# Kernel tuning notes

Hardware: AMD Instinct MI355X
Metric: run time of the kernel (lower is better)

Reference implementation:

```python
import jax, jax.numpy as jnp
import numpy as np

CODEBOOK_SIZE = 2048
LATENT_DIM = 256
COMMITMENT_BETA = 0.25
B, C, T = 16, LATENT_DIM, 2048


def setup_inputs() -> dict:
    key = jax.random.key(0)
    k1, k2 = jax.random.split(key)
    x = jax.random.normal(k1, (B, C, T), dtype=jnp.float32)
    # matches nn.Embedding.weight.data.uniform_(-1/K, 1/K)
    codebook = jax.random.uniform(
        k2, (CODEBOOK_SIZE, LATENT_DIM), dtype=jnp.float32,
        minval=-1.0 / CODEBOOK_SIZE, maxval=1.0 / CODEBOOK_SIZE)
    return {"x": x, "codebook": codebook}


def reference(x, codebook):
    b, c, t = x.shape
    # (B, C, T) -> (B*T, C)
    xf = jnp.transpose(x, (0, 2, 1)).reshape(b * t, c)
    # squared Euclidean distances; argmin is invariant to the sqrt in torch.cdist(p=2)
    x_sq = jnp.sum(xf * xf, axis=1, keepdims=True)            # (BT, 1)
    e_sq = jnp.sum(codebook * codebook, axis=1)[None, :]      # (1, K)
    d2 = x_sq - 2.0 * (xf @ codebook.T) + e_sq                # (BT, K)
    idx = jnp.argmin(d2, axis=-1)                             # (BT,)
    # gather codebook vectors -> (B, C, T)
    quant = codebook[idx].reshape(b, t, c).transpose(0, 2, 1)
    commitment_loss = COMMITMENT_BETA * jnp.mean(
        (jax.lax.stop_gradient(quant) - x) ** 2)
    codebook_loss = jnp.mean((quant - jax.lax.stop_gradient(x)) ** 2)
    # straight-through estimator
    quant_out = x + jax.lax.stop_gradient(quant - x)
    return quant_out, codebook_loss, commitment_loss, idx.reshape(b, t)
```

## Files before the change

### kernel.cpp

```cpp
#include <hip/hip_runtime.h>
#include <hip/hip_bf16.h>

#define KCODES 2048
#define DIM 256
#define TLEN 2048
#define NB 16
#define NROWS (NB * TLEN)
#define NELEM (NB * DIM * TLEN)
#define LOSS_OFF NELEM
#define IDX_OFF (NELEM + 2)

#define AMARGIN 1.8e-3f

#define CCAP 48

#define OFF_XSQ   0ull
#define OFF_ESQ   131072ull
#define OFF_KEYS  139264ull
#define OFF_BSUM  401408ull
#define OFF_EHI   532480ull
#define OFF_CCNT  1581056ull
#define OFF_CLIST 1712128ull
#define WS_NEED   8003584ull

typedef __bf16 bf16x8 __attribute__((ext_vector_type(8)));
typedef float  f32x4  __attribute__((ext_vector_type(4)));
typedef int    i32x4  __attribute__((ext_vector_type(4)));

__device__ __forceinline__ float sq_rn(float v) { return __fmul_rn(v, v); }

__device__ __forceinline__ unsigned encf(float f) {
    unsigned u = __float_as_uint(f);
    return (u & 0x80000000u) ? ~u : (u | 0x80000000u);
}
__device__ __forceinline__ float decf(unsigned k) {
    return __uint_as_float((k & 0x80000000u) ? (k & 0x7FFFFFFFu) : ~k);
}

__global__ __launch_bounds__(256) void xsq_kernel(const float* __restrict__ x,
                                                  float* __restrict__ xsq) {
    int m = blockIdx.x * 256 + threadIdx.x;
    int b = m >> 11, t = m & (TLEN - 1);
    const float* p = x + (size_t)b * DIM * TLEN + t;
    float h[2];
#pragma unroll
    for (int half = 0; half < 2; ++half) {
        int c0 = half * 128;
        float r[8];
#pragma unroll
        for (int j = 0; j < 8; ++j) r[j] = sq_rn(p[(size_t)(c0 + j) * TLEN]);
        for (int i = 8; i < 128; i += 8) {
#pragma unroll
            for (int j = 0; j < 8; ++j)
                r[j] = __fadd_rn(r[j], sq_rn(p[(size_t)(c0 + i + j) * TLEN]));
        }
        h[half] = __fadd_rn(__fadd_rn(__fadd_rn(r[0], r[1]), __fadd_rn(r[2], r[3])),
                            __fadd_rn(__fadd_rn(r[4], r[5]), __fadd_rn(r[6], r[7])));
    }
    xsq[m] = __fadd_rn(h[0], h[1]);
}

__global__ __launch_bounds__(256) void esq_kernel(const float* __restrict__ cb,
                                                  float* __restrict__ esq) {
    int k = blockIdx.x * 256 + threadIdx.x;
    const float* p = cb + (size_t)k * DIM;
    float h[2];
#pragma unroll
    for (int half = 0; half < 2; ++half) {
        int c0 = half * 128;
        float r[8];
#pragma unroll
        for (int j = 0; j < 8; ++j) r[j] = sq_rn(p[c0 + j]);
        for (int i = 8; i < 128; i += 8) {
#pragma unroll
            for (int j = 0; j < 8; ++j)
                r[j] = __fadd_rn(r[j], sq_rn(p[c0 + i + j]));
        }
        h[half] = __fadd_rn(__fadd_rn(__fadd_rn(r[0], r[1]), __fadd_rn(r[2], r[3])),
                            __fadd_rn(__fadd_rn(r[4], r[5]), __fadd_rn(r[6], r[7])));
    }
    esq[k] = __fadd_rn(h[0], h[1]);
}

__global__ __launch_bounds__(256) void prep_e_kernel(const float* __restrict__ cb,
                                                     __hip_bfloat16* __restrict__ Ehi,
                                                     float* __restrict__ esq) {
    int tid = threadIdx.x;
    int w = tid >> 6, lane = tid & 63;
    int k = (blockIdx.x << 2) + w;
    const float* p = cb + (size_t)k * DIM;

    float4 v = *reinterpret_cast<const float4*>(p + (lane << 2));
    alignas(8) __hip_bfloat16 h4[4];
    h4[0] = __float2bfloat16(v.x); h4[1] = __float2bfloat16(v.y);
    h4[2] = __float2bfloat16(v.z); h4[3] = __float2bfloat16(v.w);
    *reinterpret_cast<int2*>(Ehi + (size_t)k * DIM + (lane << 2)) = *reinterpret_cast<int2*>(h4);

    if (lane < 16) {
        int c0 = (lane >> 3) << 7, j = lane & 7;
        float r = sq_rn(p[c0 + j]);
        for (int i = 8; i < 128; i += 8)
            r = __fadd_rn(r, sq_rn(p[c0 + i + j]));
        float a  = __fadd_rn(r,  __shfl_xor(r, 1, 16));
        float b2 = __fadd_rn(a,  __shfl_xor(a, 2, 16));
        float h  = __fadd_rn(b2, __shfl_xor(b2, 4, 16));
        float tot = __fadd_rn(h, __shfl_xor(h, 8, 16));
        if (lane == 0) esq[k] = tot;
    }
}

__device__ __forceinline__ void stage_chunk(const __hip_bfloat16* __restrict__ Ehi,
                                            __hip_bfloat16* dstbase,
                                            int s, int w, int srow, int scol) {
    int ntq = s >> 3, half = (s >> 2) & 1, kc = s & 3;
    const __hip_bfloat16* gsrc =
        Ehi + (size_t)((ntq << 7) + (half << 6) + (w << 4) + srow) * DIM + (kc << 6) + scol;
#pragma unroll
    for (int j = 0; j < 2; ++j)
        __builtin_amdgcn_global_load_lds(
            (const __attribute__((address_space(1))) unsigned int*)(gsrc + (size_t)(j << 3) * DIM),
            (__attribute__((address_space(3))) unsigned int*)(dstbase + (((w << 4) + (j << 3)) << 6)),
            16, 0, 0);
}

__global__ __launch_bounds__(256, 2) void dist_cand_kernel(const float* __restrict__ x,
                                                           const __hip_bfloat16* __restrict__ Ehi,
                                                           int* __restrict__ ccnt_g,
                                                           int* __restrict__ clist_g) {
    __shared__ __hip_bfloat16 Bh[3][64 * 64];
    __shared__ unsigned short wmax16_s[64][66];
    __shared__ unsigned mask_s[64][65];
    __shared__ int ccnt_s[64];

    int tid = threadIdx.x;
    int w = tid >> 6, lane = tid & 63;
    int q = lane >> 4, c = lane & 15;
    int swzc = (c & 7) << 4;
    int blk = blockIdx.x;
    int b = blk >> 5;
    int t0 = (blk << 6) & (TLEN - 1);
    const float* xb = x + (size_t)b * DIM * TLEN + t0;

    if (tid < 64) ccnt_s[tid] = 0;

    i32x4 xf[4][8];
#pragma unroll
    for (int mi = 0; mi < 4; ++mi) {
        int t = (mi << 4) + c;
#pragma unroll
        for (int kh = 0; kh < 8; ++kh) {
            union { __hip_bfloat16 h[8]; i32x4 v; } u;
#pragma unroll
            for (int j = 0; j < 8; ++j)
                u.h[j] = __float2bfloat16(xb[(size_t)((kh << 5) + (q << 3) + j) * TLEN + t]);
            xf[mi][kh] = u.v;
            asm volatile("" : "+v"(xf[mi][kh]));
        }
    }

    f32x4 acc[2][4];
#pragma unroll
    for (int ci = 0; ci < 2; ++ci)
#pragma unroll
        for (int mi = 0; mi < 4; ++mi) acc[ci][mi] = (f32x4){0.f, 0.f, 0.f, 0.f};

    int srow = lane >> 3;
    int scol = ((lane & 7) ^ srow) << 3;

    asm volatile("s_waitcnt vmcnt(0)" ::: "memory");

    stage_chunk(Ehi, &Bh[0][0], 0, w, srow, scol);
    stage_chunk(Ehi, &Bh[1][0], 1, w, srow, scol);

    int cur = 0;
#pragma unroll 1
    for (int nt = 0; nt < 16; ++nt) {
#pragma unroll
        for (int hk = 0; hk < 8; ++hk) {
            int s = (nt << 3) + hk;
            int half = (hk >> 2) & 1;
            asm volatile("s_waitcnt lgkmcnt(0)" ::: "memory");
            int sb = cur == 0 ? 2 : cur - 1;
            if (s + 2 < 128) stage_chunk(Ehi, &Bh[sb][0], s + 2, w, srow, scol);
            if (s < 126) asm volatile("s_waitcnt vmcnt(4)" ::: "memory");
            else         asm volatile("s_waitcnt vmcnt(0)" ::: "memory");

            const char* basep = reinterpret_cast<const char*>(&Bh[cur][0]);
            int rowbyte = ((w << 4) + c) << 7;
#pragma unroll
            for (int kh = 0; kh < 2; ++kh) {
                int swz = ((kh << 6) | (q << 4)) ^ swzc;
                bf16x8 cf = *reinterpret_cast<const bf16x8*>(basep + rowbyte + swz);
#pragma unroll
                for (int mi = 0; mi < 4; ++mi) {
                    bf16x8 af = __builtin_bit_cast(bf16x8, xf[mi][((hk & 3) << 1) | kh]);
                    acc[half][mi] = __builtin_amdgcn_mfma_f32_16x16x32_bf16(cf, af, acc[half][mi], 0, 0, 0);
                }
            }
            cur = cur == 2 ? 0 : cur + 1;
        }

#pragma unroll
        for (int mi = 0; mi < 4; ++mi) {
            int r = (mi << 4) + c;
            float a8[8];
#pragma unroll
            for (int ci = 0; ci < 2; ++ci)
#pragma unroll
                for (int reg = 0; reg < 4; ++reg)
                    a8[ci * 4 + reg] = acc[ci][mi][reg];
            float m01 = fmaxf(fmaxf(a8[0], a8[1]), fmaxf(a8[2], a8[3]));
            float m23 = fmaxf(fmaxf(a8[4], a8[5]), fmaxf(a8[6], a8[7]));
            float wmax = fmaxf(m01, m23);
            wmax = fmaxf(wmax, __shfl_xor(wmax, 16, 64));
            wmax = fmaxf(wmax, __shfl_xor(wmax, 32, 64));
            float thrw = wmax - AMARGIN;
            unsigned bits = 0;
#pragma unroll
            for (int v = 0; v < 8; ++v)
                if (a8[v] >= thrw)
                    bits |= 1u << (((v >> 2) << 4) | (q << 2) | (v & 3));
            bits |= (unsigned)__shfl_xor((int)bits, 16, 64);
            bits |= (unsigned)__shfl_xor((int)bits, 32, 64);
            if (q == 0) {
                int st = (nt << 2) | w;
                wmax16_s[r][st] = (unsigned short)(encf(wmax) >> 16);
                mask_s[r][st] = bits;
            }
            acc[0][mi] = (f32x4){0.f, 0.f, 0.f, 0.f};
            acc[1][mi] = (f32x4){0.f, 0.f, 0.f, 0.f};
        }
    }

    __syncthreads();

    {
        int r = tid >> 2, j4 = tid & 3;
        int m = (blk << 6) + r;
        int g16 = 0;
#pragma unroll
        for (int i = 0; i < 16; ++i) {
            int v = wmax16_s[r][(i << 2) | j4];
            g16 = v > g16 ? v : g16;
        }
        g16 = max(g16, __shfl_xor(g16, 1, 4));
        g16 = max(g16, __shfl_xor(g16, 2, 4));
        float thr = decf((unsigned)g16 << 16) - AMARGIN;
        for (int i = 0; i < 16; ++i) {
            int st = (i << 2) | j4;
            if (decf((unsigned)wmax16_s[r][st] << 16) >= thr) {
                unsigned bits = mask_s[r][st];
                while (bits) {
                    int p = __ffs(bits) - 1; bits &= bits - 1;
                    int pos = atomicAdd(&ccnt_s[r], 1);
                    if (pos < CCAP)
                        clist_g[(size_t)m * CCAP + pos] =
                            ((st >> 2) << 7) + (((p >> 4)) << 6) + ((st & 3) << 4) + (p & 15);
                }
            }
        }
    }
    __syncthreads();
    if ((tid & 3) == 0) ccnt_g[(blk << 6) + (tid >> 2)] = ccnt_s[tid >> 2];
}

__global__ __launch_bounds__(256) void recheck_kernel(const float* __restrict__ x,
                                                      const float* __restrict__ cb,
                                                      const float* __restrict__ esq,
                                                      const int* __restrict__ ccnt,
                                                      const int* __restrict__ clist,
                                                      unsigned long long* __restrict__ keys) {
    __shared__ float xT[DIM * 33];

    int tid = threadIdx.x;
    int blk = blockIdx.x;
    int b = blk >> 6, t0 = (blk & 63) << 5;
    const float* xb = x + (size_t)b * DIM * TLEN + t0;

    {
        int tl = tid & 31, c8 = tid >> 5;
        for (int cc = 0; cc < 32; ++cc) {
            int c = (cc << 3) + c8;
            xT[c * 33 + tl] = xb[(size_t)c * TLEN + tl];
        }
    }
    __syncthreads();

    int g = tid >> 3, l3 = tid & 7;
    int m = (b << 11) + t0 + g;

    float h[2];
#pragma unroll
    for (int half = 0; half < 2; ++half) {
        int c0 = half * 128;
        float r = sq_rn(xT[(c0 + l3) * 33 + g]);
        for (int i = 8; i < 128; i += 8)
            r = __fadd_rn(r, sq_rn(xT[(c0 + i + l3) * 33 + g]));
        float a = __fadd_rn(r, __shfl_xor(r, 1, 8));
        float bb = __fadd_rn(a, __shfl_xor(a, 2, 8));
        h[half] = __fadd_rn(bb, __shfl_xor(bb, 4, 8));
    }
    float xs = __fadd_rn(h[0], h[1]);

    int cnt = ccnt[m];
    float bd = 3.4e38f; int bi = 0x7fffffff;

    if (cnt <= CCAP) {
        for (int j = l3; j < cnt; j += 8) {
            int n = clist[(size_t)m * CCAP + j];
            const float* crow = cb + (size_t)n * DIM;
            float d = 0.f;
            for (int k = 0; k < DIM; k += 4) {
                float4 cv = *reinterpret_cast<const float4*>(crow + k);
                d = fmaf(xT[(k + 0) * 33 + g], cv.x, d);
                d = fmaf(xT[(k + 1) * 33 + g], cv.y, d);
                d = fmaf(xT[(k + 2) * 33 + g], cv.z, d);
                d = fmaf(xT[(k + 3) * 33 + g], cv.w, d);
            }
            float d2 = __fadd_rn(__fadd_rn(xs, -2.0f * d), esq[n]);
            if (d2 < bd || (d2 == bd && n < bi)) { bd = d2; bi = n; }
        }
    } else {
        for (int n = l3; n < KCODES; n += 8) {
            const float* crow = cb + (size_t)n * DIM;
            float d = 0.f;
            for (int k = 0; k < DIM; k += 4) {
                float4 cv = *reinterpret_cast<const float4*>(crow + k);
                d = fmaf(xT[(k + 0) * 33 + g], cv.x, d);
                d = fmaf(xT[(k + 1) * 33 + g], cv.y, d);
                d = fmaf(xT[(k + 2) * 33 + g], cv.z, d);
                d = fmaf(xT[(k + 3) * 33 + g], cv.w, d);
            }
            float d2 = __fadd_rn(__fadd_rn(xs, -2.0f * d), esq[n]);
            if (d2 < bd || (d2 == bd && n < bi)) { bd = d2; bi = n; }
        }
    }
    for (int off = 1; off < 8; off <<= 1) {
        float od = __shfl_xor(bd, off, 8);
        int   oi = __shfl_xor(bi, off, 8);
        if (od < bd || (od == bd && oi < bi)) { bd = od; bi = oi; }
    }
    if (l3 == 0)
        keys[m] = ((unsigned long long)__float_as_uint(bd) << 32) | (unsigned)(bi & 2047);
}

__global__ __launch_bounds__(256) void init_keys_kernel(unsigned long long* __restrict__ keys) {
    keys[blockIdx.x * 256 + threadIdx.x] = ~0ULL;
}

__global__ __launch_bounds__(256, 4) void dist_kernel(const float* __restrict__ x,
                                                      const float* __restrict__ cb,
                                                      const float* __restrict__ xsq,
                                                      const float* __restrict__ esq,
                                                      unsigned long long* __restrict__ keys) {
    __shared__ float As[16][128];
    __shared__ float Bs[16][132];
    int blk = blockIdx.x;
    int nt = blk & 15, mt = blk >> 4;
    int m0 = mt << 7;
    int b = m0 >> 11, t0 = m0 & (TLEN - 1);
    int n0 = nt << 7;
    int tid = threadIdx.x;
    int tm = tid >> 4, tn = tid & 15;
    const float* xbase = x + (size_t)b * DIM * TLEN + t0;
    float acc[8][8] = {};
    for (int kk = 0; kk < DIM; kk += 16) {
#pragma unroll
        for (int h = 0; h < 2; ++h) {
            int qq = tid + (h << 8);
            int k = qq >> 5, mq = (qq & 31) << 2;
            float4 v = *reinterpret_cast<const float4*>(xbase + (size_t)(kk + k) * TLEN + mq);
            *reinterpret_cast<float4*>(&As[k][mq]) = v;
        }
#pragma unroll
        for (int h = 0; h < 2; ++h) {
            int qq = tid + (h << 8);
            int nr = qq >> 2, kc = (qq & 3) << 2;
            float4 v = *reinterpret_cast<const float4*>(cb + (size_t)(n0 + nr) * DIM + kk + kc);
            Bs[kc + 0][nr] = v.x; Bs[kc + 1][nr] = v.y;
            Bs[kc + 2][nr] = v.z; Bs[kc + 3][nr] = v.w;
        }
        __syncthreads();
#pragma unroll
        for (int k = 0; k < 16; ++k) {
            float4 a0 = *reinterpret_cast<const float4*>(&As[k][tm << 2]);
            float4 a1 = *reinterpret_cast<const float4*>(&As[k][64 + (tm << 2)]);
            float4 b0 = *reinterpret_cast<const float4*>(&Bs[k][tn << 2]);
            float4 b1 = *reinterpret_cast<const float4*>(&Bs[k][64 + (tn << 2)]);
            float am[8] = {a0.x, a0.y, a0.z, a0.w, a1.x, a1.y, a1.z, a1.w};
            float bn[8] = {b0.x, b0.y, b0.z, b0.w, b1.x, b1.y, b1.z, b1.w};
#pragma unroll
            for (int mi = 0; mi < 8; ++mi)
#pragma unroll
                for (int ni = 0; ni < 8; ++ni)
                    acc[mi][ni] = fmaf(am[mi], bn[ni], acc[mi][ni]);
        }
        __syncthreads();
    }
    int cn[8]; float es[8];
#pragma unroll
    for (int ni = 0; ni < 8; ++ni) {
        cn[ni] = n0 + ((ni < 4) ? (tn << 2) + ni : 60 + (tn << 2) + ni);
        es[ni] = esq[cn[ni]];
    }
#pragma unroll
    for (int mi = 0; mi < 8; ++mi) {
        int m = m0 + ((mi < 4) ? (tm << 2) + mi : 60 + (tm << 2) + mi);
        float xs = xsq[m];
        float bd = 3.4e38f;
        int bi = 0x7fffffff;
#pragma unroll
        for (int ni = 0; ni < 8; ++ni) {
            float d2 = __fadd_rn(__fadd_rn(xs, -2.0f * acc[mi][ni]), es[ni]);
            if (d2 < bd) { bd = d2; bi = cn[ni]; }
        }
        for (int off = 1; off < 16; off <<= 1) {
            float od = __shfl_xor(bd, off, 16);
            int oi = __shfl_xor(bi, off, 16);
            if (od < bd || (od == bd && oi < bi)) { bd = od; bi = oi; }
        }
        if (tn == 0) {
            unsigned long long key =
                ((unsigned long long)__float_as_uint(bd) << 32) | (unsigned)(bi & 2047);
            atomicMin(&keys[m], key);
        }
    }
}

__global__ __launch_bounds__(256) void gather_kernel(const float* __restrict__ x,
                                                     const float* __restrict__ cb,
                                                     const unsigned long long* __restrict__ keys,
                                                     float* __restrict__ out,
                                                     float* __restrict__ bsum) {
    int tid = threadIdx.x;
    int blk = blockIdx.x;
    int c8 = blk & 31, tc = (blk >> 5) & 7, b = blk >> 8;
    int c0 = c8 << 3;
    int t = (tc << 8) + tid;
    int m = (b << 11) + t;
    unsigned idx = (unsigned)(keys[m]) & 2047u;
    const float* crow = cb + (size_t)idx * DIM + c0;
    float4 cv0 = *reinterpret_cast<const float4*>(crow);
    float4 cv1 = *reinterpret_cast<const float4*>(crow + 4);
    if (c8 == 0) out[(size_t)IDX_OFF + m] = (float)idx;

    float qv[8] = {cv0.x, cv0.y, cv0.z, cv0.w, cv1.x, cv1.y, cv1.z, cv1.w};
    __shared__ float wsum[4][8];
    int lane = tid & 63, wid = tid >> 6;
    float sv[8];
#pragma unroll
    for (int cc = 0; cc < 8; ++cc) {
        size_t e = (size_t)b * (DIM * TLEN) + (size_t)(c0 + cc) * TLEN + t;
        float xv = x[e];
        float diff = __fsub_rn(qv[cc], xv);
        out[e] = __fadd_rn(xv, diff);
        float s = __fmul_rn(diff, diff);
        for (int off = 32; off > 0; off >>= 1) s += __shfl_down(s, off, 64);
        sv[cc] = s;
    }
    if (lane == 0) {
#pragma unroll
        for (int cc = 0; cc < 8; ++cc) wsum[wid][cc] = sv[cc];
    }
    __syncthreads();
    if (tid == 0) {
#pragma unroll
        for (int cc = 0; cc < 8; ++cc)
            bsum[(b << 11) + ((c0 + cc) << 3) + tc] =
                ((wsum[0][cc] + wsum[1][cc]) + (wsum[2][cc] + wsum[3][cc]));
    }
}

__global__ __launch_bounds__(1024) void finalize_kernel(const float* __restrict__ bsum,
                                                        float* __restrict__ out) {
    double s = 0.0;
    for (int i = threadIdx.x; i < 32768; i += 1024) s += (double)bsum[i];
    for (int off = 32; off > 0; off >>= 1) s += __shfl_down(s, off, 64);
    __shared__ double wsum[16];
    int lane = threadIdx.x & 63, wid = threadIdx.x >> 6;
    if (lane == 0) wsum[wid] = s;
    __syncthreads();
    if (threadIdx.x == 0) {
        double total = 0.0;
        for (int ww = 0; ww < 16; ++ww) total += wsum[ww];
        float mean = (float)(total / (double)NELEM);
        out[LOSS_OFF] = mean;
        out[LOSS_OFF + 1] = 0.25f * mean;
    }
}

extern "C" void kernel_launch(void* const* d_in, const int* in_sizes, int n_in,
                              void* d_out, int out_size, void* d_ws, size_t ws_size,
                              hipStream_t stream) {
    const float* x  = (const float*)d_in[0];
    const float* cb = (const float*)d_in[1];
    float* out = (float*)d_out;
    char* ws = (char*)d_ws;
    float* xsq = (float*)(ws + OFF_XSQ);
    float* esq = (float*)(ws + OFF_ESQ);
    unsigned long long* keys = (unsigned long long*)(ws + OFF_KEYS);
    float* bsum = (float*)(ws + OFF_BSUM);

    if (ws_size >= WS_NEED) {
        __hip_bfloat16* Ehi = (__hip_bfloat16*)(ws + OFF_EHI);
        int* ccnt  = (int*)(ws + OFF_CCNT);
        int* clist = (int*)(ws + OFF_CLIST);
        prep_e_kernel<<<KCODES / 4, 256, 0, stream>>>(cb, Ehi, esq);
        dist_cand_kernel<<<NROWS / 64, 256, 0, stream>>>(x, Ehi, ccnt, clist);
        recheck_kernel<<<NROWS / 32, 256, 0, stream>>>(x, cb, esq, ccnt, clist, keys);
    } else {
        esq_kernel<<<KCODES / 256, 256, 0, stream>>>(cb, esq);
        xsq_kernel<<<NROWS / 256, 256, 0, stream>>>(x, xsq);
        init_keys_kernel<<<NROWS / 256, 256, 0, stream>>>(keys);
        dist_kernel<<<(NROWS / 128) * (KCODES / 128), 256, 0, stream>>>(x, cb, xsq, esq, keys);
    }
    gather_kernel<<<(NB * 8 * 32), 256, 0, stream>>>(x, cb, keys, out, bsum);
    finalize_kernel<<<1, 1024, 0, stream>>>(bsum, out);
}
```

Before: 219.0 us.

## Restructure distance MFMA tiling: per-wave token rows, shared 64-code tiles, 4 blocks/CU

Changes the candidate-distance kernel so that each wave owns 16 tokens with the full 256-dim x held in registers. All four waves now share a 64-code by 128-dim LDS tile, where before each wave took its own 16 codes against 64 tokens. Staging now uses block-wide barriers, and the per-tile candidate masks widen to 64 bits over 32 code tiles. The smaller register footprint allows a launch bound of 4 blocks per CU, and s_setprio is raised around the MFMA loop. The cost is more LDS reads per MFMA, since codebook fragments are reloaded for every k step, plus an s_barrier on each stage.

After: 214.1 us. 2.2% less time.

```diff
diff --git a/kernel.cpp b/kernel.cpp
--- a/kernel.cpp
+++ b/kernel.cpp
@@ -110,126 +110,125 @@
 }
 
 __device__ __forceinline__ void stage_chunk(const __hip_bfloat16* __restrict__ Ehi,
-                                            __hip_bfloat16* dstbase,
-                                            int s, int w, int srow, int scol) {
-    int ntq = s >> 3, half = (s >> 2) & 1, kc = s & 3;
-    const __hip_bfloat16* gsrc =
-        Ehi + (size_t)((ntq << 7) + (half << 6) + (w << 4) + srow) * DIM + (kc << 6) + scol;
-#pragma unroll
-    for (int j = 0; j < 2; ++j)
+                                            __hip_bfloat16* dst,
+                                            int s, int w, int lane) {
+    int n0 = (s >> 1) << 6, k0 = (s & 1) << 7;
+    int rlo = lane >> 4;
+    int slot = lane & 15;
+#pragma unroll
+    for (int j = 0; j < 4; ++j) {
+        int row = (((w << 2) + j) << 2);
+        int gr = row + rlo;
+        int scol = ((slot ^ (gr & 7)) << 3);
+        const __hip_bfloat16* gsrc = Ehi + (size_t)(n0 + gr) * DIM + k0 + scol;
         __builtin_amdgcn_global_load_lds(
-            (const __attribute__((address_space(1))) unsigned int*)(gsrc + (size_t)(j << 3) * DIM),
-            (__attribute__((address_space(3))) unsigned int*)(dstbase + (((w << 4) + (j << 3)) << 6)),
+            (const __attribute__((address_space(1))) unsigned int*)gsrc,
+            (__attribute__((address_space(3))) unsigned int*)(dst + ((size_t)row << 7)),
             16, 0, 0);
-}
-
-__global__ __launch_bounds__(256, 2) void dist_cand_kernel(const float* __restrict__ x,
+    }
+}
+
+__global__ __launch_bounds__(256, 4) void dist_cand_kernel(const float* __restrict__ x,
                                                            const __hip_bfloat16* __restrict__ Ehi,
                                                            int* __restrict__ ccnt_g,
                                                            int* __restrict__ clist_g) {
-    __shared__ __hip_bfloat16 Bh[3][64 * 64];
-    __shared__ unsigned short wmax16_s[64][66];
-    __shared__ unsigned mask_s[64][65];
+    __shared__ __hip_bfloat16 Bh[3][64 * 128];
+    __shared__ unsigned short wmax16_s[64][34];
+    __shared__ unsigned long long mask_s[64][33];
     __shared__ int ccnt_s[64];
 
     int tid = threadIdx.x;
     int w = tid >> 6, lane = tid & 63;
     int q = lane >> 4, c = lane & 15;
-    int swzc = (c & 7) << 4;
     int blk = blockIdx.x;
     int b = blk >> 5;
-    int t0 = (blk << 6) & (TLEN - 1);
+    int t0 = (blk & 31) << 6;
     const float* xb = x + (size_t)b * DIM * TLEN + t0;
 
     if (tid < 64) ccnt_s[tid] = 0;
 
-    i32x4 xf[4][8];
-#pragma unroll
-    for (int mi = 0; mi < 4; ++mi) {
-        int t = (mi << 4) + c;
-#pragma unroll
-        for (int kh = 0; kh < 8; ++kh) {
-            union { __hip_bfloat16 h[8]; i32x4 v; } u;
-#pragma unroll
-            for (int j = 0; j < 8; ++j)
-                u.h[j] = __float2bfloat16(xb[(size_t)((kh << 5) + (q << 3) + j) * TLEN + t]);
-            xf[mi][kh] = u.v;
-            asm volatile("" : "+v"(xf[mi][kh]));
-        }
-    }
-
-    f32x4 acc[2][4];
-#pragma unroll
-    for (int ci = 0; ci < 2; ++ci)
-#pragma unroll
-        for (int mi = 0; mi < 4; ++mi) acc[ci][mi] = (f32x4){0.f, 0.f, 0.f, 0.f};
-
-    int srow = lane >> 3;
-    int scol = ((lane & 7) ^ srow) << 3;
+    int trow = (w << 4) + c;
+
+    i32x4 xf[8];
+#pragma unroll
+    for (int kh = 0; kh < 8; ++kh) {
+        union { __hip_bfloat16 h[8]; i32x4 v; } u;
+#pragma unroll
+        for (int j = 0; j < 8; ++j)
+            u.h[j] = __float2bfloat16(xb[(size_t)((kh << 5) + (q << 3) + j) * TLEN + trow]);
+        xf[kh] = u.v;
+        asm volatile("" : "+v"(xf[kh]));
+    }
+
+    f32x4 acc[4];
+#pragma unroll
+    for (int ci = 0; ci < 4; ++ci) acc[ci] = (f32x4){0.f, 0.f, 0.f, 0.f};
 
     asm volatile("s_waitcnt vmcnt(0)" ::: "memory");
-
-    stage_chunk(Ehi, &Bh[0][0], 0, w, srow, scol);
-    stage_chunk(Ehi, &Bh[1][0], 1, w, srow, scol);
+    __syncthreads();
+
+    stage_chunk(Ehi, &Bh[0][0], 0, w, lane);
+    stage_chunk(Ehi, &Bh[1][0], 1, w, lane);
 
     int cur = 0;
 #pragma unroll 1
-    for (int nt = 0; nt < 16; ++nt) {
-#pragma unroll
-        for (int hk = 0; hk < 8; ++hk) {
-            int s = (nt << 3) + hk;
-            int half = (hk >> 2) & 1;
-            asm volatile("s_waitcnt lgkmcnt(0)" ::: "memory");
+    for (int nt = 0; nt < 32; ++nt) {
+#pragma unroll
+        for (int kc2 = 0; kc2 < 2; ++kc2) {
+            int s = (nt << 1) + kc2;
+            asm volatile("s_barrier" ::: "memory");
             int sb = cur == 0 ? 2 : cur - 1;
-            if (s + 2 < 128) stage_chunk(Ehi, &Bh[sb][0], s + 2, w, srow, scol);
-            if (s < 126) asm volatile("s_waitcnt vmcnt(4)" ::: "memory");
-            else         asm volatile("s_waitcnt vmcnt(0)" ::: "memory");
+            if (s + 2 < 64) stage_chunk(Ehi, &Bh[sb][0], s + 2, w, lane);
+            if (s < 62)      asm volatile("s_waitcnt vmcnt(8)" ::: "memory");
+            else if (s == 62) asm volatile("s_waitcnt vmcnt(4)" ::: "memory");
+            else              asm volatile("s_waitcnt vmcnt(0)" ::: "memory");
 
             const char* basep = reinterpret_cast<const char*>(&Bh[cur][0]);
-            int rowbyte = ((w << 4) + c) << 7;
-#pragma unroll
-            for (int kh = 0; kh < 2; ++kh) {
-                int swz = ((kh << 6) | (q << 4)) ^ swzc;
-                bf16x8 cf = *reinterpret_cast<const bf16x8*>(basep + rowbyte + swz);
-#pragma unroll
-                for (int mi = 0; mi < 4; ++mi) {
-                    bf16x8 af = __builtin_bit_cast(bf16x8, xf[mi][((hk & 3) << 1) | kh]);
-                    acc[half][mi] = __builtin_amdgcn_mfma_f32_16x16x32_bf16(cf, af, acc[half][mi], 0, 0, 0);
+            __builtin_amdgcn_s_setprio(1);
+#pragma unroll
+            for (int kh4 = 0; kh4 < 4; ++kh4) {
+                bf16x8 af = __builtin_bit_cast(bf16x8, xf[(kc2 << 2) + kh4]);
+#pragma unroll
+                for (int ci = 0; ci < 4; ++ci) {
+                    int rr = (ci << 4) + c;
+                    int slot = ((kh4 << 2) | q) ^ (c & 7);
+                    bf16x8 cf = *reinterpret_cast<const bf16x8*>(basep + (rr << 8) + (slot << 4));
+                    acc[ci] = __builtin_amdgcn_mfma_f32_16x16x32_bf16(cf, af, acc[ci], 0, 0, 0);
                 }
             }
+            __builtin_amdgcn_s_setprio(0);
             cur = cur == 2 ? 0 : cur + 1;
         }
 
-#pragma unroll
-        for (int mi = 0; mi < 4; ++mi) {
-            int r = (mi << 4) + c;
-            float a8[8];
-#pragma unroll
-            for (int ci = 0; ci < 2; ++ci)
-#pragma unroll
-                for (int reg = 0; reg < 4; ++reg)
-                    a8[ci * 4 + reg] = acc[ci][mi][reg];
-            float m01 = fmaxf(fmaxf(a8[0], a8[1]), fmaxf(a8[2], a8[3]));
-            float m23 = fmaxf(fmaxf(a8[4], a8[5]), fmaxf(a8[6], a8[7]));
-            float wmax = fmaxf(m01, m23);
-            wmax = fmaxf(wmax, __shfl_xor(wmax, 16, 64));
-            wmax = fmaxf(wmax, __shfl_xor(wmax, 32, 64));
-            float thrw = wmax - AMARGIN;
-            unsigned bits = 0;
-#pragma unroll
-            for (int v = 0; v < 8; ++v)
-                if (a8[v] >= thrw)
-                    bits |= 1u << (((v >> 2) << 4) | (q << 2) | (v & 3));
-            bits |= (unsigned)__shfl_xor((int)bits, 16, 64);
-            bits |= (unsigned)__shfl_xor((int)bits, 32, 64);
-            if (q == 0) {
-                int st = (nt << 2) | w;
-                wmax16_s[r][st] = (unsigned short)(encf(wmax) >> 16);
-                mask_s[r][st] = bits;
-            }
-            acc[0][mi] = (f32x4){0.f, 0.f, 0.f, 0.f};
-            acc[1][mi] = (f32x4){0.f, 0.f, 0.f, 0.f};
-        }
+        float a16[16];
+#pragma unroll
+        for (int ci = 0; ci < 4; ++ci)
+#pragma unroll
+            for (int reg = 0; reg < 4; ++reg)
+                a16[ci * 4 + reg] = acc[ci][reg];
+        float m0 = fmaxf(fmaxf(a16[0], a16[1]), fmaxf(a16[2], a16[3]));
+        float m1 = fmaxf(fmaxf(a16[4], a16[5]), fmaxf(a16[6], a16[7]));
+        float m2 = fmaxf(fmaxf(a16[8], a16[9]), fmaxf(a16[10], a16[11]));
+        float m3 = fmaxf(fmaxf(a16[12], a16[13]), fmaxf(a16[14], a16[15]));
+        float wmax = fmaxf(fmaxf(m0, m1), fmaxf(m2, m3));
+        wmax = fmaxf(wmax, __shfl_xor(wmax, 16, 64));
+        wmax = fmaxf(wmax, __shfl_xor(wmax, 32, 64));
+        float thrw = wmax - AMARGIN;
+        unsigned long long bits = 0;
+#pragma unroll
+        for (int ci = 0; ci < 4; ++ci)
+#pragma unroll
+            for (int reg = 0; reg < 4; ++reg)
+                if (a16[ci * 4 + reg] >= thrw)
+                    bits |= 1ULL << ((ci << 4) + (q << 2) + reg);
+        bits |= (unsigned long long)__shfl_xor((long long)bits, 16, 64);
+        bits |= (unsigned long long)__shfl_xor((long long)bits, 32, 64);
+        if (q == 0) {
+            wmax16_s[trow][nt] = (unsigned short)(encf(wmax) >> 16);
+            mask_s[trow][nt] = bits;
+        }
+#pragma unroll
+        for (int ci = 0; ci < 4; ++ci) acc[ci] = (f32x4){0.f, 0.f, 0.f, 0.f};
     }
 
     __syncthreads();
@@ -239,23 +238,21 @@
         int m = (blk << 6) + r;
         int g16 = 0;
 #pragma unroll
-        for (int i = 0; i < 16; ++i) {
+        for (int i = 0; i < 8; ++i) {
             int v = wmax16_s[r][(i << 2) | j4];
             g16 = v > g16 ? v : g16;
         }
         g16 = max(g16, __shfl_xor(g16, 1, 4));
         g16 = max(g16, __shfl_xor(g16, 2, 4));
         float thr = decf((unsigned)g16 << 16) - AMARGIN;
-        for (int i = 0; i < 16; ++i) {
-            int st = (i << 2) | j4;
-            if (decf((unsigned)wmax16_s[r][st] << 16) >= thr) {
-                unsigned bits = mask_s[r][st];
+        for (int i = 0; i < 8; ++i) {
+            int nt = (i << 2) | j4;
+            if (decf((unsigned)wmax16_s[r][nt] << 16) >= thr) {
+                unsigned long long bits = mask_s[r][nt];
                 while (bits) {
-                    int p = __ffs(bits) - 1; bits &= bits - 1;
+                    int p = __ffsll((long long)bits) - 1; bits &= bits - 1;
                     int pos = atomicAdd(&ccnt_s[r], 1);
-                    if (pos < CCAP)
-                        clist_g[(size_t)m * CCAP + pos] =
-                            ((st >> 2) << 7) + (((p >> 4)) << 6) + ((st & 3) << 4) + (p & 15);
+                    if (pos < CCAP) clist_g[(size_t)m * CCAP + pos] = (nt << 6) + p;
                 }
             }
         }
```
